# Kernel tuning notes

Measured on AMD Instinct MI355X. Metric: run time of the kernel, lower is better.

The kernel has to match this reference:

```python
import jax, jax.numpy as jnp
import numpy as np

D = 256          # object_dim == query_dim
HG = 1024        # g hidden / output width
HF0, HF1 = 1024, 512
OUT_F = 256
N = 32768        # number of objects


def _mlp_g(h, W0, b0, W1, b1, W2, b2):
    # g=True: ReLU after every layer, including output.
    h = jax.nn.relu(h @ W0 + b0)
    h = jax.nn.relu(h @ W1 + b1)
    return jax.nn.relu(h @ W2 + b2)


def _mlp_f(h, W0, b0, W1, b1, W2, b2):
    # f: ReLU on hidden layers, linear output.
    h = jax.nn.relu(h @ W0 + b0)
    h = jax.nn.relu(h @ W1 + b1)
    return h @ W2 + b2


def setup_inputs() -> dict:
    key = jax.random.key(0)
    ks = jax.random.split(key, 16)
    def lin(k, fan_in, fan_out):
        s = 1.0 / np.sqrt(fan_in)
        kw, kb = jax.random.split(k)
        W = jax.random.uniform(kw, (fan_in, fan_out), jnp.float32, -s, s)
        b = jax.random.uniform(kb, (fan_out,), jnp.float32, -s, s)
        return W, b
    x = jax.random.normal(ks[0], (N, D), jnp.float32)
    q = jax.random.normal(ks[1], (D,), jnp.float32)
    g_W0, g_b0 = lin(ks[2], 3 * D, HG)
    g_W1, g_b1 = lin(ks[3], HG, HG)
    g_W2, g_b2 = lin(ks[4], HG, HG)
    f_W0, f_b0 = lin(ks[5], HG, HF0)
    f_W1, f_b1 = lin(ks[6], HF0, HF1)
    f_W2, f_b2 = lin(ks[7], HF1, OUT_F)
    return dict(x=x, q=q,
                g_W0=g_W0, g_b0=g_b0, g_W1=g_W1, g_b1=g_b1, g_W2=g_W2, g_b2=g_b2,
                f_W0=f_W0, f_b0=f_b0, f_W1=f_W1, f_b1=f_b1, f_W2=f_W2, f_b2=f_b2)


def reference(x, q, g_W0, g_b0, g_W1, g_b1, g_W2, g_b2,
              f_W0, f_b0, f_W1, f_b1, f_W2, f_b2):
    n = x.shape[0]
    # mode 4: adjacent pairs (o_i, o_{i+1}), query concatenated to each pair.
    pair_concat = jnp.concatenate(
        [x[:-1], x[1:], jnp.broadcast_to(q, (n - 1, q.shape[0]))], axis=-1)  # (n-1, 3D)
    relations = _mlp_g(pair_concat, g_W0, g_b0, g_W1, g_b1, g_W2, g_b2)       # (n-1, HG)
    embedding = jnp.sum(relations, axis=0)                                     # (HG,)
    return _mlp_f(embedding, f_W0, f_b0, f_W1, f_b1, f_W2, f_b2)               # (OUT_F,)
```

## Files before the change

### kernel.cpp

```cpp
#include <hip/hip_runtime.h>

typedef __attribute__((ext_vector_type(8))) short short8;
typedef __attribute__((ext_vector_type(4))) float floatx4;

#define NROWS 32768L
#define NVALID 32767L
#define HGDIM 1024

__device__ __forceinline__ unsigned short f2bf_rne(float f) {
    union { float f; unsigned u; } v; v.f = f;
    unsigned r = v.u + 0x7fffu + ((v.u >> 16) & 1u);
    return (unsigned short)(r >> 16);
}

__device__ __forceinline__ void gload_lds16(const void* g, void* l) {
    __builtin_amdgcn_global_load_lds(
        (const __attribute__((address_space(1))) void*)g,
        (__attribute__((address_space(3))) void*)l,
        16, 0, 0);
}

__global__ void cvt_x(const float* __restrict__ x, unsigned short* __restrict__ xb,
                      long nx, long ntot4) {
    long i = (long)blockIdx.x * 256 + threadIdx.x;
    if (i >= ntot4) return;
    long i4 = i * 4;
    float4 v = make_float4(0.f, 0.f, 0.f, 0.f);
    if (i4 < nx) v = *(const float4*)(x + i4);
    ushort4 o;
    o.x = f2bf_rne(v.x); o.y = f2bf_rne(v.y); o.z = f2bf_rne(v.z); o.w = f2bf_rne(v.w);
    *(ushort4*)(xb + i4) = o;
}

__global__ void transpose_cvt(const float* __restrict__ W, unsigned short* __restrict__ Wt,
                              int K, int N) {
    __shared__ float tile[32][33];
    int tx = threadIdx.x & 31, ty = threadIdx.x >> 5;
    int nb = blockIdx.x * 32, kb = blockIdx.y * 32;
    #pragma unroll
    for (int i = 0; i < 32; i += 8)
        tile[ty + i][tx] = W[(size_t)(kb + ty + i) * N + (nb + tx)];
    __syncthreads();
    #pragma unroll
    for (int i = 0; i < 32; i += 8)
        Wt[(size_t)(nb + ty + i) * K + (kb + tx)] = f2bf_rne(tile[tx][ty + i]);
}

template<bool RELU_IN>
__global__ void fc_partial(const float* __restrict__ in, const float* __restrict__ W,
                           const float* __restrict__ bias, float* __restrict__ out,
                           int N) {
    __shared__ float s_in[128];
    int j = blockIdx.x * 256 + threadIdx.x;
    int k0 = blockIdx.y * 128;
    if (threadIdx.x < 128) {
        float v = in[k0 + threadIdx.x];
        if (RELU_IN) v = fmaxf(v, 0.f);
        s_in[threadIdx.x] = v;
    }
    __syncthreads();
    float acc = (blockIdx.y == 0) ? bias[j] : 0.f;
    #pragma unroll 4
    for (int k = 0; k < 128; ++k)
        acc += s_in[k] * W[(size_t)(k0 + k) * N + j];
    atomicAdd(&out[j], acc);
}

template<int COLSUM>
__global__ __launch_bounds__(256, 2)
void gemm_bt(const unsigned short* __restrict__ A, int lda,
             const unsigned short* __restrict__ Bt, int ldb,
             const float* __restrict__ bias, int K,
             unsigned short* __restrict__ Hout,
             float* __restrict__ emb, long row0g, long nvalid) {
    __shared__ alignas(16) unsigned short ldsA[128 * 64];
    __shared__ alignas(16) unsigned short ldsB[128 * 64];

    const int t = threadIdx.x;
    const int lane = t & 63;
    const int wave = t >> 6;
    const int wm = wave >> 1, wn = wave & 1;
    const int m0 = blockIdx.x * 128;
    const int n0 = blockIdx.y * 128;

    floatx4 acc[4][4] = {};

    const int sr = t >> 3;
    const int spc = t & 7;

    for (int k0 = 0; k0 < K; k0 += 64) {
        #pragma unroll
        for (int i = 0; i < 4; ++i) {
            int rr = sr + 32 * i;
            int pca = spc ^ (rr & 7);
            const unsigned short* gA = A + (size_t)(m0 + rr) * lda + (k0 + pca * 8);
            gload_lds16(gA, (char*)ldsA + (rr * 128 + spc * 16));
            const unsigned short* gB = Bt + (size_t)(n0 + rr) * ldb + (k0 + pca * 8);
            gload_lds16(gB, (char*)ldsB + (rr * 128 + spc * 16));
        }
        asm volatile("s_waitcnt vmcnt(0)" ::: "memory");
        __syncthreads();

        #pragma unroll
        for (int kk = 0; kk < 2; ++kk) {
            short8 af[4], bf[4];
            #pragma unroll
            for (int mf = 0; mf < 4; ++mf) {
                int r = wm * 64 + mf * 16 + (lane & 15);
                int c = kk * 4 + (lane >> 4);
                int pc = c ^ (r & 7);
                af[mf] = *(const short8*)((const char*)ldsA + (r * 128 + pc * 16));
            }
            #pragma unroll
            for (int nf = 0; nf < 4; ++nf) {
                int r = wn * 64 + nf * 16 + (lane & 15);
                int c = kk * 4 + (lane >> 4);
                int pc = c ^ (r & 7);
                bf[nf] = *(const short8*)((const char*)ldsB + (r * 128 + pc * 16));
            }
            #pragma unroll
            for (int mf = 0; mf < 4; ++mf)
                #pragma unroll
                for (int nf = 0; nf < 4; ++nf)
                    acc[mf][nf] = __builtin_amdgcn_mfma_f32_16x16x32_bf16(
                        af[mf], bf[nf], acc[mf][nf], 0, 0, 0);
        }
        __syncthreads();
    }

    if (COLSUM == 0) {
        #pragma unroll
        for (int nf = 0; nf < 4; ++nf) {
            int ncol = n0 + wn * 64 + nf * 16 + (lane & 15);
            float bv = bias[ncol];
            #pragma unroll
            for (int mf = 0; mf < 4; ++mf) {
                int rbase = m0 + wm * 64 + mf * 16 + (lane >> 4) * 4;
                #pragma unroll
                for (int j = 0; j < 4; ++j) {
                    float v = fmaxf(acc[mf][nf][j] + bv, 0.f);
                    Hout[(size_t)(rbase + j) * HGDIM + ncol] = f2bf_rne(v);
                }
            }
        }
    } else {
        #pragma unroll
        for (int nf = 0; nf < 4; ++nf) {
            int ncol = n0 + wn * 64 + nf * 16 + (lane & 15);
            float bv = bias[ncol];
            float cs = 0.f;
            #pragma unroll
            for (int mf = 0; mf < 4; ++mf) {
                long rbase = row0g + m0 + wm * 64 + mf * 16 + (lane >> 4) * 4;
                #pragma unroll
                for (int j = 0; j < 4; ++j) {
                    float v = fmaxf(acc[mf][nf][j] + bv, 0.f);
                    if (rbase + j < nvalid) cs += v;
                }
            }
            cs += __shfl_xor(cs, 16);
            cs += __shfl_xor(cs, 32);
            if ((lane >> 4) == 0) atomicAdd(&emb[ncol], cs);
        }
    }
}

extern "C" void kernel_launch(void* const* d_in, const int* in_sizes, int n_in,
                              void* d_out, int out_size, void* d_ws, size_t ws_size,
                              hipStream_t stream) {
    const float* x   = (const float*)d_in[0];
    const float* q   = (const float*)d_in[1];
    const float* gW0 = (const float*)d_in[2];
    const float* gb0 = (const float*)d_in[3];
    const float* gW1 = (const float*)d_in[4];
    const float* gb1 = (const float*)d_in[5];
    const float* gW2 = (const float*)d_in[6];
    const float* gb2 = (const float*)d_in[7];
    const float* fW0 = (const float*)d_in[8];
    const float* fb0 = (const float*)d_in[9];
    const float* fW1 = (const float*)d_in[10];
    const float* fb1 = (const float*)d_in[11];
    const float* fW2 = (const float*)d_in[12];
    const float* fb2 = (const float*)d_in[13];
    float* out = (float*)d_out;

    char* ws = (char*)d_ws;
    size_t off = 0;
    auto alloc = [&](size_t bytes) -> char* {
        char* p = ws + off;
        off += (bytes + 255) & ~(size_t)255;
        return p;
    };
    unsigned short* xb  = (unsigned short*)alloc((NROWS + 1) * 256 * 2);
    unsigned short* w0t = (unsigned short*)alloc((size_t)1024 * 512 * 2);
    unsigned short* w1t = (unsigned short*)alloc((size_t)1024 * 1024 * 2);
    unsigned short* w2t = (unsigned short*)alloc((size_t)1024 * 1024 * 2);
    float* c0  = (float*)alloc(4096);
    float* emb = (float*)alloc(4096);
    float* e1  = (float*)alloc(4096);
    float* e2  = (float*)alloc(4096);
    size_t fixed = off;
    size_t avail = (ws_size > fixed) ? ws_size - fixed : 0;
    long CR = (long)((avail / 2) / (HGDIM * 2));
    CR = (CR / 128) * 128;
    if (CR > NROWS) CR = NROWS;
    if (CR < 128) CR = 128;
    unsigned short* H0 = (unsigned short*)alloc((size_t)CR * HGDIM * 2);
    unsigned short* H1 = (unsigned short*)alloc((size_t)CR * HGDIM * 2);

    hipMemsetAsync(c0, 0, 4 * 4096, stream);
    hipMemsetAsync(out, 0, 256 * sizeof(float), stream);

    long ntot4 = (NROWS + 1) * 256 / 4;
    cvt_x<<<dim3((unsigned)((ntot4 + 255) / 256)), 256, 0, stream>>>(x, xb, NROWS * 256, ntot4);

    transpose_cvt<<<dim3(32, 16), 256, 0, stream>>>(gW0, w0t, 512, 1024);
    transpose_cvt<<<dim3(32, 32), 256, 0, stream>>>(gW1, w1t, 1024, 1024);
    transpose_cvt<<<dim3(32, 32), 256, 0, stream>>>(gW2, w2t, 1024, 1024);

    fc_partial<false><<<dim3(4, 2), 256, 0, stream>>>(q, gW0 + (size_t)512 * 1024, gb0, c0, 1024);

    for (long r0 = 0; r0 < NROWS; r0 += CR) {
        long rows = NROWS - r0; if (rows > CR) rows = CR;
        dim3 g((unsigned)(rows / 128), 8);
        gemm_bt<0><<<g, 256, 0, stream>>>(xb + r0 * 256, 256, w0t, 512, c0, 512,
                                          H0, nullptr, 0, 0);
        gemm_bt<0><<<g, 256, 0, stream>>>(H0, 1024, w1t, 1024, gb1, 1024,
                                          H1, nullptr, 0, 0);
        gemm_bt<1><<<g, 256, 0, stream>>>(H1, 1024, w2t, 1024, gb2, 1024,
                                          nullptr, emb, r0, NVALID);
    }

    fc_partial<false><<<dim3(4, 8), 256, 0, stream>>>(emb, fW0, fb0, e1, 1024);
    fc_partial<true><<<dim3(2, 8), 256, 0, stream>>>(e1, fW1, fb1, e2, 512);
    fc_partial<true><<<dim3(1, 4), 256, 0, stream>>>(e2, fW2, fb2, out, 256);
}
```

Before: 276.9 us.

## Replace 128x128 GEMM with double-buffered 256x256 pipelined MFMA kernel

Replaces the 128x128-tile, single-buffered bf16 GEMM with a 256x256-tile, 512-thread kernel. The new kernel double-buffers LDS and interleaves global-to-LDS staging with MFMA clusters, using s_setprio and partial vmcnt waits. It also remaps workgroups in an XCD-aware swizzle for better L2 locality. The goal is to hide memory latency and raise MFMA utilisation on the three g-MLP GEMMs, at the cost of much higher register and LDS use (128 KB LDS) and fragile hand scheduling.

```diff
diff --git a/kernel.cpp b/kernel.cpp
--- a/kernel.cpp
+++ b/kernel.cpp
@@ -66,67 +66,114 @@
     atomicAdd(&out[j], acc);
 }
 
+
+#define P_PRE() do { __builtin_amdgcn_sched_barrier(0); __builtin_amdgcn_s_barrier(); \
+    asm volatile("s_waitcnt lgkmcnt(0)" ::: "memory"); __builtin_amdgcn_sched_barrier(0); \
+    __builtin_amdgcn_s_setprio(1); } while (0)
+
+#define P_POST() do { __builtin_amdgcn_s_setprio(0); __builtin_amdgcn_sched_barrier(0); \
+    __builtin_amdgcn_s_barrier(); } while (0)
+
+#define P_POSTV6() do { __builtin_amdgcn_s_setprio(0); __builtin_amdgcn_sched_barrier(0); \
+    asm volatile("s_waitcnt vmcnt(6)" ::: "memory"); __builtin_amdgcn_sched_barrier(0); \
+    __builtin_amdgcn_s_barrier(); } while (0)
+
+#define STAGE(buf, region, T) do { \
+    if ((region) >= 2) { \
+        const unsigned short* _g = gA + (long)(((region) & 1) * 128) * lda + (long)(T) * 64; \
+        char* _d = (char*)&lds[buf][0][((region) & 1) * 128][0] + t * 16; \
+        gload_lds16(_g, _d); \
+        gload_lds16(_g + 64L * lda, _d + 8192); \
+    } else { \
+        const unsigned short* _g = gB + (long)(((region) & 1) * 128) * ldb + (long)(T) * 64; \
+        char* _d = (char*)&lds[buf][1][((region) & 1) * 128][0] + t * 16; \
+        gload_lds16(_g, _d); \
+        gload_lds16(_g + 64L * ldb, _d + 8192); \
+    } } while (0)
+
+#define LDA4(dst, buf, mbase, ks) do { _Pragma("unroll") for (int _q = 0; _q < 4; ++_q) \
+    dst[_q] = *(const short8*)((const char*)&lds[buf][0][arowb + ((mbase) + _q) * 16][0] + ((ks) ? cb1 : cb0)); } while (0)
+
+#define LDB4(dst, buf, ks) do { _Pragma("unroll") for (int _q = 0; _q < 4; ++_q) \
+    dst[_q] = *(const short8*)((const char*)&lds[buf][1][browb + _q * 16][0] + ((ks) ? cb1 : cb0)); } while (0)
+
+#define MFMA16(AF, BF, MO) do { _Pragma("unroll") for (int _mf = 0; _mf < 4; ++_mf) { \
+    _Pragma("unroll") for (int _nf = 0; _nf < 4; ++_nf) \
+        acc[(MO) + _mf][_nf] = __builtin_amdgcn_mfma_f32_16x16x32_bf16(AF[_mf], BF[_nf], acc[(MO) + _mf][_nf], 0, 0, 0); } } while (0)
+
 template<int COLSUM>
-__global__ __launch_bounds__(256, 2)
-void gemm_bt(const unsigned short* __restrict__ A, int lda,
+__global__ __launch_bounds__(512, 2)
+void gemm256(const unsigned short* __restrict__ A, int lda,
              const unsigned short* __restrict__ Bt, int ldb,
              const float* __restrict__ bias, int K,
              unsigned short* __restrict__ Hout,
-             float* __restrict__ emb, long row0g, long nvalid) {
-    __shared__ alignas(16) unsigned short ldsA[128 * 64];
-    __shared__ alignas(16) unsigned short ldsB[128 * 64];
+             float* __restrict__ emb, long row0g, long nvalid,
+             int mblocks) {
+    __shared__ alignas(16) unsigned short lds[2][2][256][64];
 
     const int t = threadIdx.x;
+    int nwg = gridDim.x, bid = blockIdx.x, swz;
+    if ((nwg & 7) == 0) { int cpx = nwg >> 3; swz = (bid & 7) * cpx + (bid >> 3); }
+    else swz = bid;
+    const int mb = swz % mblocks, nb = swz / mblocks;
+    const long m0 = (long)mb * 256;
+    const int n0 = nb * 256;
+
+    const int srow = t >> 3;
+    const int ssc = (t & 7) ^ (srow & 7);
+    const unsigned short* gA = A + (m0 + srow) * (long)lda + ssc * 8;
+    const unsigned short* gB = Bt + ((long)n0 + srow) * (long)ldb + ssc * 8;
+
     const int lane = t & 63;
-    const int wave = t >> 6;
-    const int wm = wave >> 1, wn = wave & 1;
-    const int m0 = blockIdx.x * 128;
-    const int n0 = blockIdx.y * 128;
-
-    floatx4 acc[4][4] = {};
-
-    const int sr = t >> 3;
-    const int spc = t & 7;
-
-    for (int k0 = 0; k0 < K; k0 += 64) {
-        #pragma unroll
-        for (int i = 0; i < 4; ++i) {
-            int rr = sr + 32 * i;
-            int pca = spc ^ (rr & 7);
-            const unsigned short* gA = A + (size_t)(m0 + rr) * lda + (k0 + pca * 8);
-            gload_lds16(gA, (char*)ldsA + (rr * 128 + spc * 16));
-            const unsigned short* gB = Bt + (size_t)(n0 + rr) * ldb + (k0 + pca * 8);
-            gload_lds16(gB, (char*)ldsB + (rr * 128 + spc * 16));
-        }
-        asm volatile("s_waitcnt vmcnt(0)" ::: "memory");
-        __syncthreads();
-
-        #pragma unroll
-        for (int kk = 0; kk < 2; ++kk) {
-            short8 af[4], bf[4];
-            #pragma unroll
-            for (int mf = 0; mf < 4; ++mf) {
-                int r = wm * 64 + mf * 16 + (lane & 15);
-                int c = kk * 4 + (lane >> 4);
-                int pc = c ^ (r & 7);
-                af[mf] = *(const short8*)((const char*)ldsA + (r * 128 + pc * 16));
-            }
-            #pragma unroll
-            for (int nf = 0; nf < 4; ++nf) {
-                int r = wn * 64 + nf * 16 + (lane & 15);
-                int c = kk * 4 + (lane >> 4);
-                int pc = c ^ (r & 7);
-                bf[nf] = *(const short8*)((const char*)ldsB + (r * 128 + pc * 16));
-            }
-            #pragma unroll
-            for (int mf = 0; mf < 4; ++mf)
-                #pragma unroll
-                for (int nf = 0; nf < 4; ++nf)
-                    acc[mf][nf] = __builtin_amdgcn_mfma_f32_16x16x32_bf16(
-                        af[mf], bf[nf], acc[mf][nf], 0, 0, 0);
-        }
-        __syncthreads();
-    }
+    const int wv = t >> 6;
+    const int wm = wv >> 2, wn = wv & 3;
+    const int arowb = wm * 128 + (lane & 15);
+    const int browb = wn * 64 + (lane & 15);
+    const int c0x = (lane >> 4) ^ (lane & 7);
+    const int cb0 = c0x * 16;
+    const int cb1 = (c0x ^ 4) * 16;
+
+    floatx4 acc[8][4] = {};
+
+    const int NT = K >> 6;
+    const int NI = NT >> 1;
+
+    STAGE(0, 0, 0); STAGE(0, 1, 0); STAGE(0, 2, 0); STAGE(0, 3, 0);
+    STAGE(1, 0, 1); STAGE(1, 1, 1); STAGE(1, 2, 1);
+    asm volatile("s_waitcnt vmcnt(6)" ::: "memory");
+    __builtin_amdgcn_sched_barrier(0);
+    __builtin_amdgcn_s_barrier();
+
+    for (int i = 0; i < NI; ++i) {
+        const int T1 = 2 * i + 1;
+        int T2 = 2 * i + 2; if (T2 >= NT) T2 -= NT;
+        int T3 = 2 * i + 3; if (T3 >= NT) T3 -= NT;
+
+        short8 b00[4], b01[4], a0[4], a1[4], a2[4], a3[4];
+        short8 c00[4], c01[4], d0[4], d1[4], d2[4], d3[4];
+
+        LDB4(b00, 0, 0); LDB4(b01, 0, 1); LDA4(a0, 0, 0, 0);
+        STAGE(1, 3, T1);
+        P_PRE(); MFMA16(a0, b00, 0); P_POST();
+        LDA4(a1, 0, 4, 0); LDA4(a2, 0, 0, 1); LDA4(a3, 0, 4, 1);
+        STAGE(0, 0, T2);
+        P_PRE(); MFMA16(a1, b00, 4); P_POST();
+        STAGE(0, 1, T2);
+        P_PRE(); MFMA16(a2, b01, 0); P_POST();
+        STAGE(0, 2, T2);
+        P_PRE(); MFMA16(a3, b01, 4); P_POSTV6();
+        LDB4(c00, 1, 0); LDB4(c01, 1, 1); LDA4(d0, 1, 0, 0);
+        STAGE(0, 3, T2);
+        P_PRE(); MFMA16(d0, c00, 0); P_POST();
+        LDA4(d1, 1, 4, 0); LDA4(d2, 1, 0, 1); LDA4(d3, 1, 4, 1);
+        STAGE(1, 0, T3);
+        P_PRE(); MFMA16(d1, c00, 4); P_POST();
+        STAGE(1, 1, T3);
+        P_PRE(); MFMA16(d2, c01, 0); P_POST();
+        STAGE(1, 2, T3);
+        P_PRE(); MFMA16(d3, c01, 4); P_POSTV6();
+    }
+    asm volatile("s_waitcnt vmcnt(0)" ::: "memory");
 
     if (COLSUM == 0) {
         #pragma unroll
@@ -134,8 +181,8 @@
             int ncol = n0 + wn * 64 + nf * 16 + (lane & 15);
             float bv = bias[ncol];
             #pragma unroll
-            for (int mf = 0; mf < 4; ++mf) {
-                int rbase = m0 + wm * 64 + mf * 16 + (lane >> 4) * 4;
+            for (int mf = 0; mf < 8; ++mf) {
+                long rbase = m0 + wm * 128 + mf * 16 + ((lane >> 4) << 2);
                 #pragma unroll
                 for (int j = 0; j < 4; ++j) {
                     float v = fmaxf(acc[mf][nf][j] + bv, 0.f);
@@ -150,8 +197,8 @@
             float bv = bias[ncol];
             float cs = 0.f;
             #pragma unroll
-            for (int mf = 0; mf < 4; ++mf) {
-                long rbase = row0g + m0 + wm * 64 + mf * 16 + (lane >> 4) * 4;
+            for (int mf = 0; mf < 8; ++mf) {
+                long rbase = row0g + m0 + wm * 128 + mf * 16 + ((lane >> 4) << 2);
                 #pragma unroll
                 for (int j = 0; j < 4; ++j) {
                     float v = fmaxf(acc[mf][nf][j] + bv, 0.f);
@@ -202,9 +249,9 @@
     size_t fixed = off;
     size_t avail = (ws_size > fixed) ? ws_size - fixed : 0;
     long CR = (long)((avail / 2) / (HGDIM * 2));
-    CR = (CR / 128) * 128;
+    CR = (CR / 512) * 512;
     if (CR > NROWS) CR = NROWS;
-    if (CR < 128) CR = 128;
+    if (CR < 512) CR = 512;
     unsigned short* H0 = (unsigned short*)alloc((size_t)CR * HGDIM * 2);
     unsigned short* H1 = (unsigned short*)alloc((size_t)CR * HGDIM * 2);
 
@@ -222,13 +269,14 @@
 
     for (long r0 = 0; r0 < NROWS; r0 += CR) {
         long rows = NROWS - r0; if (rows > CR) rows = CR;
-        dim3 g((unsigned)(rows / 128), 8);
-        gemm_bt<0><<<g, 256, 0, stream>>>(xb + r0 * 256, 256, w0t, 512, c0, 512,
-                                          H0, nullptr, 0, 0);
-        gemm_bt<0><<<g, 256, 0, stream>>>(H0, 1024, w1t, 1024, gb1, 1024,
-                                          H1, nullptr, 0, 0);
-        gemm_bt<1><<<g, 256, 0, stream>>>(H1, 1024, w2t, 1024, gb2, 1024,
-                                          nullptr, emb, r0, NVALID);
+        int mblocks = (int)(rows / 256);
+        dim3 g((unsigned)(mblocks * 4));
+        gemm256<0><<<g, 512, 0, stream>>>(xb + r0 * 256, 256, w0t, 512, c0, 512,
+                                          H0, nullptr, 0, 0, mblocks);
+        gemm256<0><<<g, 512, 0, stream>>>(H0, 1024, w1t, 1024, gb1, 1024,
+                                          H1, nullptr, 0, 0, mblocks);
+        gemm256<1><<<g, 512, 0, stream>>>(H1, 1024, w2t, 1024, gb2, 1024,
+                                          nullptr, emb, r0, NVALID, mblocks);
     }
 
     fc_partial<false><<<dim3(4, 8), 256, 0, stream>>>(emb, fW0, fb0, e1, 1024);
```

After: 323.0 us. 1.17x slower.
